# Kernel optimization log

Hardware: AMD Instinct MI355X
Metric: run time of the kernel (lower is better)

## Reference

```python
import jax, jax.numpy as jnp
import numpy as np

MASS = 1.5
DT = 0.01      # physics.refresh_rate
EPS = 1e-6
B, STATE, ACT, T, H = 2048, 12, 4, 128, 512

_NORM = np.zeros(STATE, dtype=np.float32)
_NORM[0] = 4.0 / np.pi; _NORM[1] = 0.5; _NORM[2] = 4.0 / np.pi
_NORM[3] = 0.1; _NORM[4] = 1.0 / 60.0; _NORM[5] = 1.0 / 60.0
_NORM = jnp.asarray(_NORM)  # indices 6:12 stay zero (predict only normalizes 0:6)


def _leaky(x):
    return jnp.where(x >= 0, x, 0.01 * x)


def _mlp(x, W0, b0, W1, b1, W2, b2, W3, b3):
    # 3 hidden LeakyReLU layers + linear head (dropout is eval-mode identity)
    h = _leaky(x @ W0 + b0)
    h = _leaky(h @ W1 + b1)
    h = _leaky(h @ W2 + b2)
    return h @ W3 + b3


def _L_EB(phi, theta, psi):
    cph, sph = jnp.cos(phi), jnp.sin(phi)
    cth, sth = jnp.cos(theta), jnp.sin(theta)
    cps, sps = jnp.cos(psi), jnp.sin(psi)
    r1 = jnp.stack([cth * cps, sph * sth * cps - cph * sps, cph * sth * cps + sph * sps], -1)
    r2 = jnp.stack([cth * sps, sph * sth * sps + cph * cps, cph * sth * sps - sph * cps], -1)
    r3 = jnp.stack([-sth, sph * cth, cph * cth], -1)
    return jnp.stack([r1, r2, r3], -2)  # [B,3,3]


def _derivs(x, forces, I_mat, I_inv):
    V = x[:, 3:6]
    phi, theta = x[:, 6], x[:, 7]
    psi = x[:, 8]
    omega = x[:, 9:12]
    Fv, M = forces[:, 0:3], forces[:, 3:6]
    dpos = jnp.einsum('bij,bj->bi', _L_EB(phi, theta, psi), V)
    dvel = Fv / MASS - jnp.cross(omega, V)
    tth = jnp.tan(theta)
    cth = jnp.clip(jnp.cos(theta), EPS)
    sph, cph = jnp.sin(phi), jnp.cos(phi)
    one, zero = jnp.ones_like(phi), jnp.zeros_like(phi)
    J = jnp.stack([
        jnp.stack([one, sph * tth, cph * tth], -1),
        jnp.stack([zero, cph, -sph], -1),
        jnp.stack([zero, sph / cth, cph / cth], -1)], -2)  # [B,3,3]
    datt = jnp.einsum('bij,bj->bi', J, omega)
    Iw = omega @ I_mat.T                       # I @ omega
    coriolis = jnp.cross(omega, Iw)
    domega = (M - coriolis) @ I_inv.T
    return jnp.concatenate([dpos, dvel, datt, domega], axis=1)


def _rk4(x, forces, I_mat, I_inv):
    f = lambda s: _derivs(s, forces, I_mat, I_inv)
    k1 = f(x)
    k2 = f(x + 0.5 * DT * k1)
    k3 = f(x + 0.5 * DT * k2)
    k4 = f(x + DT * k3)
    return x + (DT / 6.0) * (k1 + 2 * k2 + 2 * k3 + k4)


def _predict(x, act, W, I_mat, I_inv):
    norm_x = x * _NORM
    norm_act = (act - 1500.0) / 500.0
    fn = _mlp(jnp.concatenate([norm_x, norm_act], axis=1), *W)
    zeros = jnp.zeros_like(fn[:, 0])
    forces = jnp.stack([fn[:, 0] - 0.5,
                        fn[:, 1] * -0.4 - 10.0,
                        fn[:, 2] * 0.2 - 0.1,
                        zeros, zeros, zeros], axis=1)
    return forces, _rk4(x, forces, I_mat, I_inv)


def setup_inputs() -> dict:
    key = jax.random.key(0)
    ks = jax.random.split(key, 12)
    x_t = jax.random.normal(ks[0], (B, STATE), dtype=jnp.float32) * 0.1
    act_inps = jax.random.uniform(ks[1], (B, ACT, T), dtype=jnp.float32,
                                  minval=1000.0, maxval=2000.0)
    I_mat = jnp.asarray([[0.02, 0.001, 0.002],
                         [0.001, 0.03, 0.001],
                         [0.002, 0.001, 0.04]], dtype=jnp.float32)
    def lin(k, fi, fo):
        s = np.sqrt(2.0 / (fi + fo)).astype(np.float32)
        return jax.random.normal(k, (fi, fo), dtype=jnp.float32) * s
    dims = [(STATE + ACT, H), (H, H), (H, H), (H, 6)]
    W = {}
    for i, (fi, fo) in enumerate(dims):
        W[f'W{i}'] = lin(ks[2 + i], fi, fo)
        W[f'b{i}'] = jnp.zeros((fo,), dtype=jnp.float32)
    return dict(x_t=x_t, act_inps=act_inps, I_mat=I_mat, seq_len=T, **W)


def reference(x_t, act_inps, I_mat, W0, b0, W1, b1, W2, b2, W3, b3, seq_len):
    I_inv = jnp.linalg.inv(I_mat)
    W = (W0, b0, W1, b1, W2, b2, W3, b3)
    acts = jnp.transpose(act_inps[:, :, 1:seq_len], (2, 0, 1))  # [T-1,B,ACT]

    def step(x, act):
        forces, nx = _predict(x, act, W, I_mat, I_inv)
        return nx, (forces, nx)

    _, (forces_seq, x_seq) = jax.lax.scan(step, x_t, acts)
    stacked = jnp.concatenate([x_t[:, :, None], jnp.transpose(x_seq, (1, 2, 0))], axis=2)  # [B,12,T]
    stackedForces = jnp.transpose(forces_seq, (1, 2, 0))  # [B,6,T-1]
    return stackedForces, stacked
```

## Files before the change

### kernel.cpp

```cpp
#include <hip/hip_runtime.h>
#include <stdint.h>

typedef unsigned short u16;
typedef unsigned int   u32;
typedef __attribute__((ext_vector_type(8))) short short8;
typedef __attribute__((ext_vector_type(4))) float f32x4;

#define B_TOT   2048
#define HID     512
#define T_FULL  128
#define ROWS    32
#define NWG     (B_TOT / ROWS)
#define THREADS 512
#define NT      4

#define W0F_SZ  16384
#define W1F_SZ  262144
#define W3F_SZ  8192
#define WF_TOTAL (W0F_SZ + 2*W1F_SZ + W3F_SZ)

__device__ __forceinline__ u16 f2bf(float f){
  u32 u = __float_as_uint(f);
  u32 r = (u + 0x7FFFu + ((u >> 16) & 1u)) >> 16;
  return (u16)r;
}

__device__ __forceinline__ int lds_idx(int m, int k){
  int chunk = k >> 3;
  return m * 512 + ((chunk ^ (m & 7)) << 3) + (k & 7);
}

__global__ void wm_repack(const float* __restrict__ W0, const float* __restrict__ W1,
                          const float* __restrict__ W2, const float* __restrict__ W3,
                          u16* __restrict__ wf)
{
  int idx = blockIdx.x * blockDim.x + threadIdx.x;
  if (idx >= WF_TOTAL) return;
  int e = idx;
  if (e < W0F_SZ){
    int j = e & 7, l = (e >> 3) & 63, nt = e >> 9;
    int k = ((l >> 4) << 3) + j, n = (nt << 4) + (l & 15);
    wf[idx] = (k < 16) ? f2bf(W0[k * HID + n]) : (u16)0;
    return;
  }
  e -= W0F_SZ;
  if (e < W1F_SZ){
    int j = e & 7, l = (e >> 3) & 63, rest = e >> 9, kt = rest & 15, nt = rest >> 4;
    int k = (kt << 5) + ((l >> 4) << 3) + j, n = (nt << 4) + (l & 15);
    wf[idx] = f2bf(W1[k * HID + n]);
    return;
  }
  e -= W1F_SZ;
  if (e < W1F_SZ){
    int j = e & 7, l = (e >> 3) & 63, rest = e >> 9, kt = rest & 15, nt = rest >> 4;
    int k = (kt << 5) + ((l >> 4) << 3) + j, n = (nt << 4) + (l & 15);
    wf[idx] = f2bf(W2[k * HID + n]);
    return;
  }
  e -= W1F_SZ;
  {
    int j = e & 7, l = (e >> 3) & 63, kt = e >> 9;
    int k = (kt << 5) + ((l >> 4) << 3) + j, n = l & 15;
    wf[idx] = (n < 6) ? f2bf(W3[k * 6 + n]) : (u16)0;
  }
}

__device__ __forceinline__ void invert3(const float* a, float* inv){
  float d = a[0]*(a[4]*a[8]-a[5]*a[7]) - a[1]*(a[3]*a[8]-a[5]*a[6]) + a[2]*(a[3]*a[7]-a[4]*a[6]);
  float id = 1.0f / d;
  inv[0]=(a[4]*a[8]-a[5]*a[7])*id; inv[1]=(a[2]*a[7]-a[1]*a[8])*id; inv[2]=(a[1]*a[5]-a[2]*a[4])*id;
  inv[3]=(a[5]*a[6]-a[3]*a[8])*id; inv[4]=(a[0]*a[8]-a[2]*a[6])*id; inv[5]=(a[2]*a[3]-a[0]*a[5])*id;
  inv[6]=(a[3]*a[7]-a[4]*a[6])*id; inv[7]=(a[1]*a[6]-a[0]*a[7])*id; inv[8]=(a[0]*a[4]-a[1]*a[3])*id;
}

__device__ __forceinline__ void derivs(const float* x, const float* Fv,
                                       const float* I9, const float* Ii, float* dx)
{
  float V0=x[3], V1=x[4], V2=x[5];
  float phi=x[6], th=x[7], psi=x[8];
  float w0=x[9], w1=x[10], w2=x[11];
  float sph=__sinf(phi), cph=__cosf(phi);
  float sth=__sinf(th),  cth=__cosf(th);
  float sps=__sinf(psi), cps=__cosf(psi);
  float r00=cth*cps, r01=sph*sth*cps - cph*sps, r02=cph*sth*cps + sph*sps;
  float r10=cth*sps, r11=sph*sth*sps + cph*cps, r12=cph*sth*sps - sph*cps;
  float r20=-sth,    r21=sph*cth,               r22=cph*cth;
  dx[0]=r00*V0+r01*V1+r02*V2;
  dx[1]=r10*V0+r11*V1+r12*V2;
  dx[2]=r20*V0+r21*V1+r22*V2;
  const float invm = 1.0f/1.5f;
  dx[3]=Fv[0]*invm - (w1*V2 - w2*V1);
  dx[4]=Fv[1]*invm - (w2*V0 - w0*V2);
  dx[5]=Fv[2]*invm - (w0*V1 - w1*V0);
  float tth = sth / cth;
  float rc  = 1.0f / fmaxf(cth, 1e-6f);
  dx[6]= w0 + sph*tth*w1 + cph*tth*w2;
  dx[7]=      cph*w1     - sph*w2;
  dx[8]=      sph*rc*w1  + cph*rc*w2;
  float Iw0=I9[0]*w0+I9[1]*w1+I9[2]*w2;
  float Iw1=I9[3]*w0+I9[4]*w1+I9[5]*w2;
  float Iw2=I9[6]*w0+I9[7]*w1+I9[8]*w2;
  float c0=w1*Iw2-w2*Iw1, c1=w2*Iw0-w0*Iw2, c2=w0*Iw1-w1*Iw0;
  dx[9] = -(Ii[0]*c0+Ii[1]*c1+Ii[2]*c2);
  dx[10]= -(Ii[3]*c0+Ii[4]*c1+Ii[5]*c2);
  dx[11]= -(Ii[6]*c0+Ii[7]*c1+Ii[8]*c2);
}

__device__ __forceinline__ void rk4(float* X, const float* Fv, const float* I9, const float* Ii){
  float k1[12],k2[12],k3[12],k4[12],xt[12];
  derivs(X,Fv,I9,Ii,k1);
  #pragma unroll
  for (int c=0;c<12;++c) xt[c]=X[c]+0.005f*k1[c];
  derivs(xt,Fv,I9,Ii,k2);
  #pragma unroll
  for (int c=0;c<12;++c) xt[c]=X[c]+0.005f*k2[c];
  derivs(xt,Fv,I9,Ii,k3);
  #pragma unroll
  for (int c=0;c<12;++c) xt[c]=X[c]+0.01f*k3[c];
  derivs(xt,Fv,I9,Ii,k4);
  #pragma unroll
  for (int c=0;c<12;++c) X[c]+=(0.01f/6.0f)*(k1[c]+2.0f*k2[c]+2.0f*k3[c]+k4[c]);
}

__device__ __forceinline__ void build_input(u16* bufA, const float* X,
                                            const float* __restrict__ act,
                                            int b, int r, int t)
{
  float vin[16];
  vin[0]=X[0]*1.2732395447351628f;
  vin[1]=X[1]*0.5f;
  vin[2]=X[2]*1.2732395447351628f;
  vin[3]=X[3]*0.1f;
  vin[4]=X[4]*0.016666666666666666f;
  vin[5]=X[5]*0.016666666666666666f;
  #pragma unroll
  for (int c=6;c<12;++c) vin[c]=0.0f;
  #pragma unroll
  for (int a=0;a<4;++a)
    vin[12+a] = (act[(size_t)(b*4+a)*T_FULL + t] - 1500.0f) * 0.002f;
  #pragma unroll
  for (int p=0;p<16;++p){
    u32 pack = 0u;
    if (p < 8) pack = (u32)f2bf(vin[2*p]) | ((u32)f2bf(vin[2*p+1]) << 16);
    ((u32*)bufA)[lds_idx(r, 2*p) >> 1] = pack;
  }
}

template<int KT>
__device__ __forceinline__ void do_layer(const u16* __restrict__ bufIn,
                                         const u16* __restrict__ wfrag,
                                         const float* __restrict__ bias,
                                         u16* __restrict__ bufOut,
                                         int lane, int ntb)
{
  const int lm = lane & 15, half = lane >> 4;
  const int m0 = lm, m1 = 16 + lm;
  const int sw0 = m0 & 7, sw1 = m1 & 7;
  f32x4 acc0[NT], acc1[NT];
  #pragma unroll
  for (int i=0;i<NT;++i){ acc0[i]=(f32x4)0.0f; acc1[i]=(f32x4)0.0f; }

  const u16* wbase = wfrag + (((size_t)ntb*KT*64 + lane) << 3);

  if constexpr (KT == 1){
    short8 A0 = *(const short8*)(bufIn + m0*512 + ((half ^ sw0) << 3));
    short8 A1 = *(const short8*)(bufIn + m1*512 + ((half ^ sw1) << 3));
    short8 Bf[NT];
    #pragma unroll
    for (int i=0;i<NT;++i)
      Bf[i] = *(const short8*)(wbase + ((size_t)i << 9));
    #pragma unroll
    for (int i=0;i<NT;++i){
      acc0[i] = __builtin_amdgcn_mfma_f32_16x16x32_bf16(A0, Bf[i], acc0[i], 0, 0, 0);
      acc1[i] = __builtin_amdgcn_mfma_f32_16x16x32_bf16(A1, Bf[i], acc1[i], 0, 0, 0);
    }
  } else {
    static_assert(KT == 16, "KT must be 1 or 16");
    short8 Bf[2][4][NT];
    #pragma unroll
    for (int j=0;j<4;++j)
      #pragma unroll
      for (int i=0;i<NT;++i)
        Bf[0][j][i] = *(const short8*)(wbase + ((size_t)(i*KT + j) << 9));
    #pragma unroll
    for (int blk=0; blk<4; ++blk){
      const int cur = blk & 1, nxt = cur ^ 1;
      if (blk < 3){
        #pragma unroll
        for (int j=0;j<4;++j)
          #pragma unroll
          for (int i=0;i<NT;++i)
            Bf[nxt][j][i] = *(const short8*)(wbase + ((size_t)(i*KT + blk*4 + 4 + j) << 9));
      }
      short8 A0[4], A1[4];
      #pragma unroll
      for (int j=0;j<4;++j){
        const int cb = ((blk*4 + j) << 2) + half;
        A0[j] = *(const short8*)(bufIn + m0*512 + ((cb ^ sw0) << 3));
        A1[j] = *(const short8*)(bufIn + m1*512 + ((cb ^ sw1) << 3));
      }
      #pragma unroll
      for (int j=0;j<4;++j)
        #pragma unroll
        for (int i=0;i<NT;++i){
          acc0[i] = __builtin_amdgcn_mfma_f32_16x16x32_bf16(A0[j], Bf[cur][j][i], acc0[i], 0, 0, 0);
          acc1[i] = __builtin_amdgcn_mfma_f32_16x16x32_bf16(A1[j], Bf[cur][j][i], acc1[i], 0, 0, 0);
        }
    }
  }
  #pragma unroll
  for (int i=0;i<NT;++i){
    int n = ((ntb + i) << 4) + lm;
    float bv = bias[n];
    #pragma unroll
    for (int reg=0; reg<4; ++reg){
      int r0 = (half << 2) + reg, r1 = 16 + r0;
      float v0 = acc0[i][reg] + bv; v0 = (v0 >= 0.0f) ? v0 : 0.01f*v0;
      float v1 = acc1[i][reg] + bv; v1 = (v1 >= 0.0f) ? v1 : 0.01f*v1;
      bufOut[lds_idx(r0, n)] = f2bf(v0);
      bufOut[lds_idx(r1, n)] = f2bf(v1);
    }
  }
}

__global__ __launch_bounds__(THREADS, 2)
void wm_main(const float* __restrict__ x_t, const float* __restrict__ act,
             const float* __restrict__ Imat, const int* __restrict__ seqlen_p,
             const float* __restrict__ b0, const float* __restrict__ b1,
             const float* __restrict__ b2, const float* __restrict__ b3,
             const u16* __restrict__ wf, float* __restrict__ out)
{
  __shared__ u16 bufA[16384];
  __shared__ u16 bufB[16384];
  float* fscr = (float*)(bufA + 256);
  const int tid  = threadIdx.x;
  const int lane = tid & 63;
  const int wave = tid >> 6;
  const int ntb  = wave * NT;
  const int rowbase = blockIdx.x * ROWS;
  const int steps = seqlen_p[0] - 1;
  const int seqlen = steps + 1;

  const u16* w0f = wf;
  const u16* w1f = wf + W0F_SZ;
  const u16* w2f = w1f + W1F_SZ;
  const u16* w3f = w2f + W1F_SZ;

  float* outF = out;
  float* outX = out + (size_t)B_TOT * 6 * steps;

  float X[12];
  if (tid < ROWS){
    const int b = rowbase + tid;
    #pragma unroll
    for (int c=0;c<12;++c){
      float raw = x_t[b*12 + c];
      X[c] = raw;
      outX[(size_t)(b*12 + c)*seqlen] = raw;
    }
    build_input(bufA, X, act, b, tid, 1);
  }

  for (int s=0; s<steps; ++s){
    __syncthreads();
    do_layer<1 >(bufA, w0f, b0, bufB, lane, ntb);
    __syncthreads();
    do_layer<16>(bufB, w1f, b1, bufA, lane, ntb);
    __syncthreads();
    do_layer<16>(bufA, w2f, b2, bufB, lane, ntb);
    __syncthreads();
    if (wave == 0){
      const int lm = lane & 15, half = lane >> 4;
      const int m0 = lm, m1 = 16 + lm;
      const int sw0 = m0 & 7, sw1 = m1 & 7;
      short8 w3r[16];
      #pragma unroll
      for (int kt=0; kt<16; ++kt)
        w3r[kt] = *(const short8*)(w3f + (((size_t)kt*64 + lane) << 3));
      f32x4 a3_0 = (f32x4)0.0f, a3_1 = (f32x4)0.0f;
      #pragma unroll
      for (int kt=0; kt<16; ++kt){
        int cb = (kt << 2) + half;
        short8 x0 = *(const short8*)(bufB + m0*512 + ((cb ^ sw0) << 3));
        short8 x1 = *(const short8*)(bufB + m1*512 + ((cb ^ sw1) << 3));
        a3_0 = __builtin_amdgcn_mfma_f32_16x16x32_bf16(x0, w3r[kt], a3_0, 0, 0, 0);
        a3_1 = __builtin_amdgcn_mfma_f32_16x16x32_bf16(x1, w3r[kt], a3_1, 0, 0, 0);
      }
      const int c = lm;
      float bv = (c < 6) ? b3[c] : 0.0f;
      #pragma unroll
      for (int mt=0; mt<2; ++mt){
        #pragma unroll
        for (int reg=0; reg<4; ++reg){
          int rr = (mt << 4) + (half << 2) + reg;
          float fn = ((mt == 0) ? a3_0[reg] : a3_1[reg]) + bv;
          float f;
          if      (c == 0) f = fn - 0.5f;
          else if (c == 1) f = fn * -0.4f - 10.0f;
          else if (c == 2) f = fn * 0.2f - 0.1f;
          else             f = 0.0f;
          if (c < 6){
            int b = rowbase + rr;
            outF[(size_t)(b*6 + c)*steps + s] = f;
          }
          if (c < 3) fscr[rr*3 + c] = f;
        }
      }
      asm volatile("s_waitcnt lgkmcnt(0)" ::: "memory");
      if (tid < ROWS){
        const int b = rowbase + tid;
        float I9[9], Ii[9];
        #pragma unroll
        for (int i=0;i<9;++i) I9[i] = Imat[i];
        invert3(I9, Ii);
        float Fv[3] = { fscr[tid*3], fscr[tid*3+1], fscr[tid*3+2] };
        rk4(X, Fv, I9, Ii);
        #pragma unroll
        for (int cc=0;cc<12;++cc)
          outX[(size_t)(b*12 + cc)*seqlen + (s+1)] = X[cc];
        if (s + 1 < steps) build_input(bufA, X, act, b, tid, s + 2);
      }
    }
  }
}

extern "C" void kernel_launch(void* const* d_in, const int* in_sizes, int n_in,
                              void* d_out, int out_size, void* d_ws, size_t ws_size,
                              hipStream_t stream)
{
  const float* x_t  = (const float*)d_in[0];
  const float* act  = (const float*)d_in[1];
  const float* Imat = (const float*)d_in[2];
  const int*   seqp = (const int*)d_in[3];
  const float* W0   = (const float*)d_in[4];
  const float* b0   = (const float*)d_in[5];
  const float* W1   = (const float*)d_in[6];
  const float* b1   = (const float*)d_in[7];
  const float* W2   = (const float*)d_in[8];
  const float* b2   = (const float*)d_in[9];
  const float* W3   = (const float*)d_in[10];
  const float* b3   = (const float*)d_in[11];
  u16* wfrag = (u16*)d_ws;

  hipLaunchKernelGGL(wm_repack, dim3((WF_TOTAL + 255)/256), dim3(256), 0, stream,
                     W0, W1, W2, W3, wfrag);
  hipLaunchKernelGGL(wm_main, dim3(NWG), dim3(THREADS), 0, stream,
                     x_t, act, Imat, seqp, b0, b1, b2, b3, wfrag, (float*)d_out);
}
```

Measured before the change: 5.598 ms.

## Stream hidden-layer weights through per-wave LDS ring via global_load_lds DMA

The two 512x512 layers no longer prefetch weight fragments into registers with a double buffer. Each wave now streams them into its own 8-slot LDS ring using global_load_lds, paced by explicit vmcnt waits, and reads each fragment back from LDS just before its MFMA. Bias values for all layers are loaded once into registers before the time loop instead of on every step. The aim is to cut VGPR pressure and keep a deeper stream of weight loads in flight. The cost is an extra 64KB of shared memory per block, which likely stops two blocks fitting per CU, plus a fine-grained, hand-counted vmcnt pipeline.

```diff
diff --git a/kernel.cpp b/kernel.cpp
--- a/kernel.cpp
+++ b/kernel.cpp
@@ -18,6 +18,16 @@
 #define W1F_SZ  262144
 #define W3F_SZ  8192
 #define WF_TOTAL (W0F_SZ + 2*W1F_SZ + W3F_SZ)
+
+typedef const __attribute__((address_space(1))) void* gas_t;
+typedef __attribute__((address_space(3))) void*       las_t;
+
+__device__ __forceinline__ void dma16(const void* g, void* l){
+  __builtin_amdgcn_global_load_lds((gas_t)g, (las_t)l, 16, 0, 0);
+}
+template<int N> __device__ __forceinline__ void wait_vm(){
+  asm volatile("s_waitcnt vmcnt(%0)" :: "n"(N) : "memory");
+}
 
 __device__ __forceinline__ u16 f2bf(float f){
   u32 u = __float_as_uint(f);
@@ -146,12 +156,12 @@
   }
 }
 
-template<int KT>
-__device__ __forceinline__ void do_layer(const u16* __restrict__ bufIn,
-                                         const u16* __restrict__ wfrag,
-                                         const float* __restrict__ bias,
-                                         u16* __restrict__ bufOut,
-                                         int lane, int ntb)
+__device__ __forceinline__ void do_layer512(const u16* __restrict__ bufIn,
+                                            const u16* __restrict__ wfragL,
+                                            const float* bv,
+                                            u16* __restrict__ bufOut,
+                                            u16* __restrict__ ring,
+                                            int lane, int ntb)
 {
   const int lm = lane & 15, half = lane >> 4;
   const int m0 = lm, m1 = 16 + lm;
@@ -160,63 +170,99 @@
   #pragma unroll
   for (int i=0;i<NT;++i){ acc0[i]=(f32x4)0.0f; acc1[i]=(f32x4)0.0f; }
 
-  const u16* wbase = wfrag + (((size_t)ntb*KT*64 + lane) << 3);
-
-  if constexpr (KT == 1){
-    short8 A0 = *(const short8*)(bufIn + m0*512 + ((half ^ sw0) << 3));
-    short8 A1 = *(const short8*)(bufIn + m1*512 + ((half ^ sw1) << 3));
-    short8 Bf[NT];
+  const u16* gl = wfragL + (size_t)lane * 8;
+
+  wait_vm<0>();
+  #pragma unroll
+  for (int c=0;c<8;++c){
+    int nt = c & 3, kt = c >> 2;
+    dma16(gl + (((size_t)(ntb + nt)*16 + kt) << 9), ring + (c << 9));
+  }
+
+  for (int kt=0; kt<14; ++kt){
+    const int cb = (kt << 2) + half;
+    short8 A0 = *(const short8*)(bufIn + m0*512 + ((cb ^ sw0) << 3));
+    short8 A1 = *(const short8*)(bufIn + m1*512 + ((cb ^ sw1) << 3));
     #pragma unroll
-    for (int i=0;i<NT;++i)
-      Bf[i] = *(const short8*)(wbase + ((size_t)i << 9));
-    #pragma unroll
-    for (int i=0;i<NT;++i){
-      acc0[i] = __builtin_amdgcn_mfma_f32_16x16x32_bf16(A0, Bf[i], acc0[i], 0, 0, 0);
-      acc1[i] = __builtin_amdgcn_mfma_f32_16x16x32_bf16(A1, Bf[i], acc1[i], 0, 0, 0);
+    for (int i=0;i<4;++i){
+      const int c = (kt << 2) + i;
+      wait_vm<7>();
+      short8 bfr = *(const short8*)(ring + ((c & 7) << 9) + lane*8);
+      acc0[i] = __builtin_amdgcn_mfma_f32_16x16x32_bf16(A0, bfr, acc0[i], 0, 0, 0);
+      acc1[i] = __builtin_amdgcn_mfma_f32_16x16x32_bf16(A1, bfr, acc1[i], 0, 0, 0);
+      const int cn = c + 8;
+      dma16(gl + (((size_t)(ntb + (cn & 3))*16 + (cn >> 2)) << 9), ring + ((c & 7) << 9));
     }
-  } else {
-    static_assert(KT == 16, "KT must be 1 or 16");
-    short8 Bf[2][4][NT];
-    #pragma unroll
-    for (int j=0;j<4;++j)
-      #pragma unroll
-      for (int i=0;i<NT;++i)
-        Bf[0][j][i] = *(const short8*)(wbase + ((size_t)(i*KT + j) << 9));
-    #pragma unroll
-    for (int blk=0; blk<4; ++blk){
-      const int cur = blk & 1, nxt = cur ^ 1;
-      if (blk < 3){
-        #pragma unroll
-        for (int j=0;j<4;++j)
-          #pragma unroll
-          for (int i=0;i<NT;++i)
-            Bf[nxt][j][i] = *(const short8*)(wbase + ((size_t)(i*KT + blk*4 + 4 + j) << 9));
-      }
-      short8 A0[4], A1[4];
-      #pragma unroll
-      for (int j=0;j<4;++j){
-        const int cb = ((blk*4 + j) << 2) + half;
-        A0[j] = *(const short8*)(bufIn + m0*512 + ((cb ^ sw0) << 3));
-        A1[j] = *(const short8*)(bufIn + m1*512 + ((cb ^ sw1) << 3));
-      }
-      #pragma unroll
-      for (int j=0;j<4;++j)
-        #pragma unroll
-        for (int i=0;i<NT;++i){
-          acc0[i] = __builtin_amdgcn_mfma_f32_16x16x32_bf16(A0[j], Bf[cur][j][i], acc0[i], 0, 0, 0);
-          acc1[i] = __builtin_amdgcn_mfma_f32_16x16x32_bf16(A1[j], Bf[cur][j][i], acc1[i], 0, 0, 0);
-        }
-    }
-  }
+  }
+#define WM_CONSUME(c, i, A0v, A1v) { \
+    short8 bfr = *(const short8*)(ring + (((c) & 7) << 9) + lane*8); \
+    acc0[i] = __builtin_amdgcn_mfma_f32_16x16x32_bf16(A0v, bfr, acc0[i], 0, 0, 0); \
+    acc1[i] = __builtin_amdgcn_mfma_f32_16x16x32_bf16(A1v, bfr, acc1[i], 0, 0, 0); }
+  {
+    const int cb = (14 << 2) + half;
+    short8 A0 = *(const short8*)(bufIn + m0*512 + ((cb ^ sw0) << 3));
+    short8 A1 = *(const short8*)(bufIn + m1*512 + ((cb ^ sw1) << 3));
+    wait_vm<7>(); WM_CONSUME(56, 0, A0, A1);
+    wait_vm<6>(); WM_CONSUME(57, 1, A0, A1);
+    wait_vm<5>(); WM_CONSUME(58, 2, A0, A1);
+    wait_vm<4>(); WM_CONSUME(59, 3, A0, A1);
+  }
+  {
+    const int cb = (15 << 2) + half;
+    short8 A0 = *(const short8*)(bufIn + m0*512 + ((cb ^ sw0) << 3));
+    short8 A1 = *(const short8*)(bufIn + m1*512 + ((cb ^ sw1) << 3));
+    wait_vm<3>(); WM_CONSUME(60, 0, A0, A1);
+    wait_vm<2>(); WM_CONSUME(61, 1, A0, A1);
+    wait_vm<1>(); WM_CONSUME(62, 2, A0, A1);
+    wait_vm<0>(); WM_CONSUME(63, 3, A0, A1);
+  }
+#undef WM_CONSUME
   #pragma unroll
   for (int i=0;i<NT;++i){
     int n = ((ntb + i) << 4) + lm;
-    float bv = bias[n];
     #pragma unroll
     for (int reg=0; reg<4; ++reg){
       int r0 = (half << 2) + reg, r1 = 16 + r0;
-      float v0 = acc0[i][reg] + bv; v0 = (v0 >= 0.0f) ? v0 : 0.01f*v0;
-      float v1 = acc1[i][reg] + bv; v1 = (v1 >= 0.0f) ? v1 : 0.01f*v1;
+      float v0 = acc0[i][reg] + bv[i]; v0 = (v0 >= 0.0f) ? v0 : 0.01f*v0;
+      float v1 = acc1[i][reg] + bv[i]; v1 = (v1 >= 0.0f) ? v1 : 0.01f*v1;
+      bufOut[lds_idx(r0, n)] = f2bf(v0);
+      bufOut[lds_idx(r1, n)] = f2bf(v1);
+    }
+  }
+}
+
+__device__ __forceinline__ void do_layer0(const u16* __restrict__ bufIn,
+                                          const u16* __restrict__ wfragL,
+                                          const float* bv,
+                                          u16* __restrict__ bufOut,
+                                          int lane, int ntb)
+{
+  const int lm = lane & 15, half = lane >> 4;
+  const int m0 = lm, m1 = 16 + lm;
+  const int sw0 = m0 & 7, sw1 = m1 & 7;
+  f32x4 acc0[NT], acc1[NT];
+  #pragma unroll
+  for (int i=0;i<NT;++i){ acc0[i]=(f32x4)0.0f; acc1[i]=(f32x4)0.0f; }
+  short8 A0 = *(const short8*)(bufIn + m0*512 + ((half ^ sw0) << 3));
+  short8 A1 = *(const short8*)(bufIn + m1*512 + ((half ^ sw1) << 3));
+  const u16* wbase = wfragL + (((size_t)ntb*64 + lane) << 3);
+  short8 Bf[NT];
+  #pragma unroll
+  for (int i=0;i<NT;++i)
+    Bf[i] = *(const short8*)(wbase + ((size_t)i << 9));
+  #pragma unroll
+  for (int i=0;i<NT;++i){
+    acc0[i] = __builtin_amdgcn_mfma_f32_16x16x32_bf16(A0, Bf[i], acc0[i], 0, 0, 0);
+    acc1[i] = __builtin_amdgcn_mfma_f32_16x16x32_bf16(A1, Bf[i], acc1[i], 0, 0, 0);
+  }
+  #pragma unroll
+  for (int i=0;i<NT;++i){
+    int n = ((ntb + i) << 4) + lm;
+    #pragma unroll
+    for (int reg=0; reg<4; ++reg){
+      int r0 = (half << 2) + reg, r1 = 16 + r0;
+      float v0 = acc0[i][reg] + bv[i]; v0 = (v0 >= 0.0f) ? v0 : 0.01f*v0;
+      float v1 = acc1[i][reg] + bv[i]; v1 = (v1 >= 0.0f) ? v1 : 0.01f*v1;
       bufOut[lds_idx(r0, n)] = f2bf(v0);
       bufOut[lds_idx(r1, n)] = f2bf(v1);
     }
@@ -232,7 +278,9 @@
 {
   __shared__ u16 bufA[16384];
   __shared__ u16 bufB[16384];
+  __shared__ u16 wring[8 * 8 * 512];
   float* fscr = (float*)(bufA + 256);
+
   const int tid  = threadIdx.x;
   const int lane = tid & 63;
   const int wave = tid >> 6;
@@ -240,6 +288,7 @@
   const int rowbase = blockIdx.x * ROWS;
   const int steps = seqlen_p[0] - 1;
   const int seqlen = steps + 1;
+  u16* myring = wring + (wave << 12);
 
   const u16* w0f = wf;
   const u16* w1f = wf + W0F_SZ;
@@ -248,6 +297,15 @@
 
   float* outF = out;
   float* outX = out + (size_t)B_TOT * 6 * steps;
+
+  const int lm0 = lane & 15;
+  float bvL0[NT], bvL1[NT], bvL2[NT];
+  #pragma unroll
+  for (int i=0;i<NT;++i){
+    int n = ((ntb + i) << 4) + lm0;
+    bvL0[i] = b0[n]; bvL1[i] = b1[n]; bvL2[i] = b2[n];
+  }
+  float bv3 = (lm0 < 6) ? b3[lm0] : 0.0f;
 
   float X[12];
   if (tid < ROWS){
@@ -263,11 +321,11 @@
 
   for (int s=0; s<steps; ++s){
     __syncthreads();
-    do_layer<1 >(bufA, w0f, b0, bufB, lane, ntb);
+    do_layer0(bufA, w0f, bvL0, bufB, lane, ntb);
     __syncthreads();
-    do_layer<16>(bufB, w1f, b1, bufA, lane, ntb);
+    do_layer512(bufB, w1f, bvL1, bufA, myring, lane, ntb);
     __syncthreads();
-    do_layer<16>(bufA, w2f, b2, bufB, lane, ntb);
+    do_layer512(bufA, w2f, bvL2, bufB, myring, lane, ntb);
     __syncthreads();
     if (wave == 0){
       const int lm = lane & 15, half = lane >> 4;
@@ -287,7 +345,7 @@
         a3_1 = __builtin_amdgcn_mfma_f32_16x16x32_bf16(x1, w3r[kt], a3_1, 0, 0, 0);
       }
       const int c = lm;
-      float bv = (c < 6) ? b3[c] : 0.0f;
+      float bv = bv3;
       #pragma unroll
       for (int mt=0; mt<2; ++mt){
         #pragma unroll
```

New measurement: 6.455 ms. 15.3% more time.

## Stream hidden-layer weights through a rolling register prefetch ring across layers

Applied to the files above, without the earlier changes.

Replaces the per-layer double-buffered weight loads with a 4-deep ring of inline-asm global loads that waits with explicit vmcnt. The ring carries over layer boundaries, so the first weight tiles of the next layer (W2 after W1, W1 of the next step after W2) are already in flight during the barrier and the output-head phase. W0 fragments, biases and the inertia inverse are also hoisted into registers outside the time loop, and __syncthreads is swapped for an LDS-only wait plus barrier. This raises register pressure and depends on hand-set vmcnt counts being correct around the other global memory traffic.

```diff
diff --git a/kernel.cpp b/kernel.cpp
--- a/kernel.cpp
+++ b/kernel.cpp
@@ -146,12 +146,27 @@
   }
 }
 
-template<int KT>
-__device__ __forceinline__ void do_layer(const u16* __restrict__ bufIn,
-                                         const u16* __restrict__ wfrag,
-                                         const float* __restrict__ bias,
-                                         u16* __restrict__ bufOut,
-                                         int lane, int ntb)
+__device__ __forceinline__ void bar_lds(){
+  asm volatile("s_waitcnt lgkmcnt(0)\n\ts_barrier" ::: "memory");
+}
+
+__device__ __forceinline__ void issue_g(short8* d, const u16* lbase, int ntb, int kt){
+  #pragma unroll
+  for (int i=0;i<4;++i){
+    const u16* p = lbase + (((size_t)((ntb + i)*16 + kt)) << 9);
+    asm volatile("global_load_dwordx4 %0, %1, off" : "=v"(d[i]) : "v"(p));
+  }
+}
+#define WAITG(g) asm volatile("s_waitcnt vmcnt(12)" \
+  : "+v"((g)[0]), "+v"((g)[1]), "+v"((g)[2]), "+v"((g)[3]))
+
+__device__ __forceinline__ void do_layer512(const u16* __restrict__ bufIn,
+                                            const u16* __restrict__ lbase,
+                                            const u16* __restrict__ nbase,
+                                            const float* bv,
+                                            u16* __restrict__ bufOut,
+                                            short8 (*bf)[4],
+                                            int lane, int ntb)
 {
   const int lm = lane & 15, half = lane >> 4;
   const int m0 = lm, m1 = 16 + lm;
@@ -160,63 +175,29 @@
   #pragma unroll
   for (int i=0;i<NT;++i){ acc0[i]=(f32x4)0.0f; acc1[i]=(f32x4)0.0f; }
 
-  const u16* wbase = wfrag + (((size_t)ntb*KT*64 + lane) << 3);
-
-  if constexpr (KT == 1){
-    short8 A0 = *(const short8*)(bufIn + m0*512 + ((half ^ sw0) << 3));
-    short8 A1 = *(const short8*)(bufIn + m1*512 + ((half ^ sw1) << 3));
-    short8 Bf[NT];
+  #pragma unroll
+  for (int kt=0; kt<16; ++kt){
+    short8* g = bf[kt & 3];
+    WAITG(g);
+    const int cb = (kt << 2) + half;
+    short8 A0 = *(const short8*)(bufIn + m0*512 + ((cb ^ sw0) << 3));
+    short8 A1 = *(const short8*)(bufIn + m1*512 + ((cb ^ sw1) << 3));
     #pragma unroll
-    for (int i=0;i<NT;++i)
-      Bf[i] = *(const short8*)(wbase + ((size_t)i << 9));
-    #pragma unroll
-    for (int i=0;i<NT;++i){
-      acc0[i] = __builtin_amdgcn_mfma_f32_16x16x32_bf16(A0, Bf[i], acc0[i], 0, 0, 0);
-      acc1[i] = __builtin_amdgcn_mfma_f32_16x16x32_bf16(A1, Bf[i], acc1[i], 0, 0, 0);
-    }
-  } else {
-    static_assert(KT == 16, "KT must be 1 or 16");
-    short8 Bf[2][4][NT];
-    #pragma unroll
-    for (int j=0;j<4;++j)
-      #pragma unroll
-      for (int i=0;i<NT;++i)
-        Bf[0][j][i] = *(const short8*)(wbase + ((size_t)(i*KT + j) << 9));
-    #pragma unroll
-    for (int blk=0; blk<4; ++blk){
-      const int cur = blk & 1, nxt = cur ^ 1;
-      if (blk < 3){
-        #pragma unroll
-        for (int j=0;j<4;++j)
-          #pragma unroll
-          for (int i=0;i<NT;++i)
-            Bf[nxt][j][i] = *(const short8*)(wbase + ((size_t)(i*KT + blk*4 + 4 + j) << 9));
-      }
-      short8 A0[4], A1[4];
-      #pragma unroll
-      for (int j=0;j<4;++j){
-        const int cb = ((blk*4 + j) << 2) + half;
-        A0[j] = *(const short8*)(bufIn + m0*512 + ((cb ^ sw0) << 3));
-        A1[j] = *(const short8*)(bufIn + m1*512 + ((cb ^ sw1) << 3));
-      }
-      #pragma unroll
-      for (int j=0;j<4;++j)
-        #pragma unroll
-        for (int i=0;i<NT;++i){
-          acc0[i] = __builtin_amdgcn_mfma_f32_16x16x32_bf16(A0[j], Bf[cur][j][i], acc0[i], 0, 0, 0);
-          acc1[i] = __builtin_amdgcn_mfma_f32_16x16x32_bf16(A1[j], Bf[cur][j][i], acc1[i], 0, 0, 0);
-        }
-    }
+    for (int i=0;i<4;++i){
+      acc0[i] = __builtin_amdgcn_mfma_f32_16x16x32_bf16(A0, g[i], acc0[i], 0, 0, 0);
+      acc1[i] = __builtin_amdgcn_mfma_f32_16x16x32_bf16(A1, g[i], acc1[i], 0, 0, 0);
+    }
+    if (kt < 12) issue_g(g, lbase, ntb, kt + 4);
+    else         issue_g(g, nbase, ntb, kt - 12);
   }
   #pragma unroll
   for (int i=0;i<NT;++i){
     int n = ((ntb + i) << 4) + lm;
-    float bv = bias[n];
     #pragma unroll
     for (int reg=0; reg<4; ++reg){
       int r0 = (half << 2) + reg, r1 = 16 + r0;
-      float v0 = acc0[i][reg] + bv; v0 = (v0 >= 0.0f) ? v0 : 0.01f*v0;
-      float v1 = acc1[i][reg] + bv; v1 = (v1 >= 0.0f) ? v1 : 0.01f*v1;
+      float v0 = acc0[i][reg] + bv[i]; v0 = (v0 >= 0.0f) ? v0 : 0.01f*v0;
+      float v1 = acc1[i][reg] + bv[i]; v1 = (v1 >= 0.0f) ? v1 : 0.01f*v1;
       bufOut[lds_idx(r0, n)] = f2bf(v0);
       bufOut[lds_idx(r1, n)] = f2bf(v1);
     }
@@ -233,6 +214,7 @@
   __shared__ u16 bufA[16384];
   __shared__ u16 bufB[16384];
   float* fscr = (float*)(bufA + 256);
+
   const int tid  = threadIdx.x;
   const int lane = tid & 63;
   const int wave = tid >> 6;
@@ -245,11 +227,30 @@
   const u16* w1f = wf + W0F_SZ;
   const u16* w2f = w1f + W1F_SZ;
   const u16* w3f = w2f + W1F_SZ;
+  const u16* w1l = w1f + (size_t)lane * 8;
+  const u16* w2l = w2f + (size_t)lane * 8;
 
   float* outF = out;
   float* outX = out + (size_t)B_TOT * 6 * steps;
 
+  const int lm0 = lane & 15;
+  short8 w0r[NT];
+  float bvL0[NT], bvL1[NT], bvL2[NT];
+  #pragma unroll
+  for (int i=0;i<NT;++i){
+    w0r[i] = *(const short8*)(w0f + (((size_t)(ntb + i)*64 + lane) << 3));
+    int n = ((ntb + i) << 4) + lm0;
+    bvL0[i] = b0[n]; bvL1[i] = b1[n]; bvL2[i] = b2[n];
+  }
+  float bv3 = (lm0 < 6) ? b3[lm0] : 0.0f;
+  float I9[9], Ii[9];
+  #pragma unroll
+  for (int i=0;i<9;++i) I9[i] = Imat[i];
+  invert3(I9, Ii);
+
   float X[12];
+  #pragma unroll
+  for (int c=0;c<12;++c) X[c] = 0.0f;
   if (tid < ROWS){
     const int b = rowbase + tid;
     #pragma unroll
@@ -260,15 +261,55 @@
     }
     build_input(bufA, X, act, b, tid, 1);
   }
+  #pragma unroll
+  for (int i=0;i<NT;++i){
+    asm volatile("" : "+v"(w0r[i]));
+    asm volatile("" : "+v"(bvL0[i]), "+v"(bvL1[i]), "+v"(bvL2[i]));
+  }
+  asm volatile("" : "+v"(bv3));
+  #pragma unroll
+  for (int i=0;i<9;++i) asm volatile("" : "+v"(I9[i]), "+v"(Ii[i]));
+  #pragma unroll
+  for (int c=0;c<12;++c) asm volatile("" : "+v"(X[c]));
+
+  short8 bf[4][4];
+  #pragma unroll
+  for (int g=0; g<4; ++g) issue_g(bf[g], w1l, ntb, g);
 
   for (int s=0; s<steps; ++s){
-    __syncthreads();
-    do_layer<1 >(bufA, w0f, b0, bufB, lane, ntb);
-    __syncthreads();
-    do_layer<16>(bufB, w1f, b1, bufA, lane, ntb);
-    __syncthreads();
-    do_layer<16>(bufA, w2f, b2, bufB, lane, ntb);
-    __syncthreads();
+    bar_lds();
+    {
+      const int lm = lane & 15, half = lane >> 4;
+      const int m0 = lm, m1 = 16 + lm;
+      const int sw0 = m0 & 7, sw1 = m1 & 7;
+      short8 A0 = *(const short8*)(bufA + m0*512 + ((half ^ sw0) << 3));
+      short8 A1 = *(const short8*)(bufA + m1*512 + ((half ^ sw1) << 3));
+      f32x4 a0[NT], a1[NT];
+      #pragma unroll
+      for (int i=0;i<NT;++i){ a0[i]=(f32x4)0.0f; a1[i]=(f32x4)0.0f; }
+      #pragma unroll
+      for (int i=0;i<NT;++i){
+        a0[i] = __builtin_amdgcn_mfma_f32_16x16x32_bf16(A0, w0r[i], a0[i], 0, 0, 0);
+        a1[i] = __builtin_amdgcn_mfma_f32_16x16x32_bf16(A1, w0r[i], a1[i], 0, 0, 0);
+      }
+      #pragma unroll
+      for (int i=0;i<NT;++i){
+        int n = ((ntb + i) << 4) + lm;
+        #pragma unroll
+        for (int reg=0; reg<4; ++reg){
+          int r0 = (half << 2) + reg, r1 = 16 + r0;
+          float v0 = a0[i][reg] + bvL0[i]; v0 = (v0 >= 0.0f) ? v0 : 0.01f*v0;
+          float v1 = a1[i][reg] + bvL0[i]; v1 = (v1 >= 0.0f) ? v1 : 0.01f*v1;
+          bufB[lds_idx(r0, n)] = f2bf(v0);
+          bufB[lds_idx(r1, n)] = f2bf(v1);
+        }
+      }
+    }
+    bar_lds();
+    do_layer512(bufB, w1l, w2l, bvL1, bufA, bf, lane, ntb);
+    bar_lds();
+    do_layer512(bufA, w2l, w1l, bvL2, bufB, bf, lane, ntb);
+    bar_lds();
     if (wave == 0){
       const int lm = lane & 15, half = lane >> 4;
       const int m0 = lm, m1 = 16 + lm;
@@ -287,13 +328,12 @@
         a3_1 = __builtin_amdgcn_mfma_f32_16x16x32_bf16(x1, w3r[kt], a3_1, 0, 0, 0);
       }
       const int c = lm;
-      float bv = (c < 6) ? b3[c] : 0.0f;
       #pragma unroll
       for (int mt=0; mt<2; ++mt){
         #pragma unroll
         for (int reg=0; reg<4; ++reg){
           int rr = (mt << 4) + (half << 2) + reg;
-          float fn = ((mt == 0) ? a3_0[reg] : a3_1[reg]) + bv;
+          float fn = ((mt == 0) ? a3_0[reg] : a3_1[reg]) + bv3;
           float f;
           if      (c == 0) f = fn - 0.5f;
           else if (c == 1) f = fn * -0.4f - 10.0f;
@@ -309,10 +349,6 @@
       asm volatile("s_waitcnt lgkmcnt(0)" ::: "memory");
       if (tid < ROWS){
         const int b = rowbase + tid;
-        float I9[9], Ii[9];
-        #pragma unroll
-        for (int i=0;i<9;++i) I9[i] = Imat[i];
-        invert3(I9, Ii);
         float Fv[3] = { fscr[tid*3], fscr[tid*3+1], fscr[tid*3+2] };
         rk4(X, Fv, I9, Ii);
         #pragma unroll
```

Measured after the change: 7.392 ms. 32.0% more time.
